# Kernel optimization log

Hardware: AMD Instinct MI355X
Metric: run time of the kernel (lower is better)

## Reference

```python
import jax, jax.numpy as jnp
import numpy as np

N_NODES = 50000
N_HYPEREDGES = 20000


def _segment_softmax(logits, seg, num_segments):
    mx = jax.ops.segment_max(logits, seg, num_segments=num_segments)
    mx = jnp.where(jnp.isfinite(mx), mx, 0.0)
    e = jnp.exp(logits - mx[seg])
    s = jax.ops.segment_sum(e, seg, num_segments=num_segments)
    return e / (s[seg] + 1e-16)


def _hypergraph_conv(x, he_node, he_edge, W, bias, num_nodes, num_he):
    # PyG HypergraphConv (use_attention=False, heads=1, hyperedge_weight=1):
    # out = D^{-1} H B^{-1} H^T (x W) + bias
    h = x @ W  # [N, C]
    ones = jnp.ones_like(he_node, dtype=h.dtype)
    D = jax.ops.segment_sum(ones, he_node, num_segments=num_nodes)
    Dinv = jnp.where(D > 0, 1.0 / D, 0.0)
    B = jax.ops.segment_sum(ones, he_edge, num_segments=num_he)
    Binv = jnp.where(B > 0, 1.0 / B, 0.0)
    # node -> hyperedge
    m = Binv[:, None] * jax.ops.segment_sum(h[he_node], he_edge, num_segments=num_he)
    # hyperedge -> node
    out = Dinv[:, None] * jax.ops.segment_sum(m[he_edge], he_node, num_segments=num_nodes)
    return out + bias


def _gat_conv(x, edge_index, W, a_src, a_dst, bias, num_nodes):
    # PyG GATConv defaults: heads=1, concat=True, slope=0.2, add_self_loops=True
    loops = jnp.arange(num_nodes)
    src = jnp.concatenate([edge_index[0], loops])
    dst = jnp.concatenate([edge_index[1], loops])
    h = x @ W  # [N, C]
    asrc = h @ a_src  # [N]
    adst = h @ a_dst  # [N]
    logit = jax.nn.leaky_relu(asrc[src] + adst[dst], negative_slope=0.2)
    alpha = _segment_softmax(logit, dst, num_nodes)  # softmax over incoming edges
    out = jax.ops.segment_sum(alpha[:, None] * h[src], dst, num_segments=num_nodes)
    return out + bias


def _mlp(e, Wm1, bm1, Wm2, bm2, Wm3, bm3, Wm4, bm4):
    # PyG MLP(128,64,3, num_layers=4) in eval mode: BN is identity at init,
    # dropout inactive -> Linear+ReLU chain, final Linear plain.
    h = jax.nn.relu(e @ Wm1 + bm1)
    h = jax.nn.relu(h @ Wm2 + bm2)
    h = jax.nn.relu(h @ Wm3 + bm3)
    return h @ Wm4 + bm4


def setup_inputs() -> dict:
    key = jax.random.key(0)
    ks = jax.random.split(key, 32)
    s = 0.05
    inp = {
        'x': jax.random.normal(ks[0], (N_NODES, 128), dtype=jnp.float32),
        'edge_index': jax.random.randint(ks[1], (2, 800000), 0, N_NODES),
        'he_node': jax.random.randint(ks[2], (400000,), 0, N_NODES),
        'he_edge': jax.random.randint(ks[3], (400000,), 0, N_HYPEREDGES),
        'edge_label_index': jax.random.randint(ks[4], (2, 100000), 0, N_NODES),
        'W1': jax.random.normal(ks[5], (128, 256)) * s,
        'b1': jnp.zeros((256,), jnp.float32),
        'W2': jax.random.normal(ks[6], (256, 256)) * s,
        'a2s': jax.random.normal(ks[7], (256,)) * s,
        'a2d': jax.random.normal(ks[8], (256,)) * s,
        'b2': jnp.zeros((256,), jnp.float32),
        'W3': jax.random.normal(ks[9], (256, 64)) * s,
        'a3s': jax.random.normal(ks[10], (64,)) * s,
        'a3d': jax.random.normal(ks[11], (64,)) * s,
        'b3': jnp.zeros((64,), jnp.float32),
        'Wm1': jax.random.normal(ks[12], (128, 64)) * s,
        'bm1': jnp.zeros((64,), jnp.float32),
        'Wm2': jax.random.normal(ks[13], (64, 64)) * s,
        'bm2': jnp.zeros((64,), jnp.float32),
        'Wm3': jax.random.normal(ks[14], (64, 64)) * s,
        'bm3': jnp.zeros((64,), jnp.float32),
        'Wm4': jax.random.normal(ks[15], (64, 3)) * s,
        'bm4': jnp.zeros((3,), jnp.float32),
    }
    return inp


def reference(x, edge_index, he_node, he_edge, edge_label_index,
              W1, b1, W2, a2s, a2d, b2, W3, a3s, a3d, b3,
              Wm1, bm1, Wm2, bm2, Wm3, bm3, Wm4, bm4):
    n = x.shape[0]
    # encode
    h = jax.nn.relu(_hypergraph_conv(x, he_node, he_edge, W1, b1, n, N_HYPEREDGES))
    h = jax.nn.relu(_gat_conv(h, edge_index, W2, a2s, a2d, b2, n))
    z = jax.nn.relu(_gat_conv(h, edge_index, W3, a3s, a3d, b3, n))
    # decode
    src, dst = edge_label_index[0], edge_label_index[1]
    edge_attr = jnp.concatenate([z[src], z[dst]], axis=-1)  # [L, 128]
    out = _mlp(edge_attr, Wm1, bm1, Wm2, bm2, Wm3, bm3, Wm4, bm4)  # [L, 3]
    out_pred = jnp.argmax(out, axis=-1)
    out_prob = jnp.take_along_axis(out, out_pred[:, None], axis=-1)[:, 0]
    return (out_pred, out_prob, out)
```

## Files before the change

### kernel.cpp

```cpp
#include <hip/hip_runtime.h>
#include <math.h>

#define NHE_CONST 20000

typedef float v4f __attribute__((ext_vector_type(4)));

__device__ __forceinline__ float lrelu(float x){ return x >= 0.f ? x : 0.2f * x; }

__global__ void k_count_all(const int* __restrict__ he_node, const int* __restrict__ he_edge, int inc,
                            const int* __restrict__ dst, int e,
                            int* cntN, int* cntHE, int* cntD){
  int i = blockIdx.x * blockDim.x + threadIdx.x;
  if (i < inc){ atomicAdd(&cntN[he_node[i]], 1); atomicAdd(&cntHE[he_edge[i]], 1); }
  if (i < e) atomicAdd(&cntD[dst[i]], 1);
}

__global__ __launch_bounds__(256) void k_scan_sums3(
    const int* __restrict__ p0, int n0, int* __restrict__ b0,
    const int* __restrict__ p1, int n1, int* __restrict__ b1,
    const int* __restrict__ p2, int n2, int* __restrict__ b2){
  const int* p; int n; int* bs;
  if (blockIdx.y == 0){ p = p0; n = n0; bs = b0; }
  else if (blockIdx.y == 1){ p = p1; n = n1; bs = b1; }
  else { p = p2; n = n2; bs = b2; }
  int nb = (n + 1023) / 1024;
  if ((int)blockIdx.x >= nb) return;
  __shared__ int sm[256];
  int base = blockIdx.x * 1024;
  int v = 0;
  for (int i = threadIdx.x; i < 1024; i += 256){
    int idx = base + i;
    v += (idx < n) ? p[idx] : 0;
  }
  sm[threadIdx.x] = v; __syncthreads();
  for (int d = 128; d > 0; d >>= 1){
    if (threadIdx.x < d) sm[threadIdx.x] += sm[threadIdx.x + d];
    __syncthreads();
  }
  if (threadIdx.x == 0) bs[blockIdx.x] = sm[0];
}

__global__ void k_scan_bsum3(int* b0, int nb0, int* b1, int nb1, int* b2, int nb2){
  int t = threadIdx.x;
  int* bs; int nb;
  if (t == 0){ bs = b0; nb = nb0; }
  else if (t == 1){ bs = b1; nb = nb1; }
  else if (t == 2){ bs = b2; nb = nb2; }
  else return;
  int acc = 0;
  for (int i = 0; i < nb; i++){ int v = bs[i]; bs[i] = acc; acc += v; }
}

__global__ __launch_bounds__(256) void k_scan_apply3(
    const int* __restrict__ c0, int n0, const int* __restrict__ s0, int* __restrict__ o0, int* __restrict__ u0,
    const int* __restrict__ c1, int n1, const int* __restrict__ s1, int* __restrict__ o1, int* __restrict__ u1,
    const int* __restrict__ c2, int n2, const int* __restrict__ s2, int* __restrict__ o2, int* __restrict__ u2){
  const int* cnt; int n; const int* bsum; int* off; int* cur;
  if (blockIdx.y == 0){ cnt = c0; n = n0; bsum = s0; off = o0; cur = u0; }
  else if (blockIdx.y == 1){ cnt = c1; n = n1; bsum = s1; off = o1; cur = u1; }
  else { cnt = c2; n = n2; bsum = s2; off = o2; cur = u2; }
  int nb = (n + 1023) / 1024;
  int b = blockIdx.x;
  if (b >= nb) return;
  __shared__ int sm[256];
  int base = b * 1024 + threadIdx.x * 4;
  int v[4];
  #pragma unroll
  for (int i = 0; i < 4; i++) v[i] = (base + i < n) ? cnt[base + i] : 0;
  int s = v[0] + v[1] + v[2] + v[3];
  sm[threadIdx.x] = s; __syncthreads();
  int x = s;
  for (int d = 1; d < 256; d <<= 1){
    int t = (threadIdx.x >= d) ? sm[threadIdx.x - d] : 0;
    __syncthreads();
    x += t; sm[threadIdx.x] = x;
    __syncthreads();
  }
  int run = x - s + bsum[b];
  #pragma unroll
  for (int i = 0; i < 4; i++){
    if (base + i < n) cur[base + i] = run;
    run += v[i];
    if (base + i < n) off[base + i + 1] = run;
  }
  if (b == 0 && threadIdx.x == 0) off[0] = 0;
}

__global__ void k_fill_all(const int* __restrict__ he_node, const int* __restrict__ he_edge, int inc,
                           const int* __restrict__ src, const int* __restrict__ dst, int e,
                           int* curN, int* curHE, int* curD,
                           int* __restrict__ nHEs, int* __restrict__ heNodes, int* __restrict__ srcIdx){
  int i = blockIdx.x * blockDim.x + threadIdx.x;
  if (i < inc){
    int nd = he_node[i], he = he_edge[i];
    int p = atomicAdd(&curHE[he], 1); heNodes[p] = nd;
    int q = atomicAdd(&curN[nd], 1);  nHEs[q]    = he;
  }
  if (i < e){ int p = atomicAdd(&curD[dst[i]], 1); srcIdx[p] = src[i]; }
}

__global__ __launch_bounds__(256) void k_gemm128_bias_relu(
    const float* __restrict__ A, const float* __restrict__ B, float* __restrict__ C,
    int M, int N, int K, const float* __restrict__ bias){
  __shared__ float As[16][132];
  __shared__ float Bs[16][128];
  int tid = threadIdx.x;
  int tn = tid & 15, tm = tid >> 4;
  int bm = blockIdx.x * 128, bn = blockIdx.y * 128;

  float acc[8][8];
  #pragma unroll
  for (int i = 0; i < 8; i++)
    #pragma unroll
    for (int j = 0; j < 8; j++) acc[i][j] = 0.f;

  int arow = tid >> 2, akc = (tid & 3) * 4;
  int brow = tid >> 4, bcol = (tid & 15) * 8;

  for (int k0 = 0; k0 < K; k0 += 16){
    #pragma unroll
    for (int h = 0; h < 2; h++){
      int r = arow + h * 64;
      int gr = bm + r;
      float4 av = (gr < M) ? *(const float4*)(A + (size_t)gr * K + k0 + akc)
                           : make_float4(0.f, 0.f, 0.f, 0.f);
      As[akc + 0][r] = av.x; As[akc + 1][r] = av.y;
      As[akc + 2][r] = av.z; As[akc + 3][r] = av.w;
    }
    const float* bp = B + (size_t)(k0 + brow) * N + bn + bcol;
    *(float4*)&Bs[brow][bcol]     = *(const float4*)bp;
    *(float4*)&Bs[brow][bcol + 4] = *(const float4*)(bp + 4);
    __syncthreads();

    #pragma unroll
    for (int k = 0; k < 16; k++){
      float4 a0 = *(const float4*)&As[k][tm * 8];
      float4 a1 = *(const float4*)&As[k][tm * 8 + 4];
      float4 b0 = *(const float4*)&Bs[k][tn * 8];
      float4 b1 = *(const float4*)&Bs[k][tn * 8 + 4];
      float a[8] = {a0.x, a0.y, a0.z, a0.w, a1.x, a1.y, a1.z, a1.w};
      float bb[8] = {b0.x, b0.y, b0.z, b0.w, b1.x, b1.y, b1.z, b1.w};
      #pragma unroll
      for (int i = 0; i < 8; i++)
        #pragma unroll
        for (int j = 0; j < 8; j++) acc[i][j] += a[i] * bb[j];
    }
    __syncthreads();
  }
  const float* bvp = bias + bn + tn * 8;
  float4 bb0 = *(const float4*)bvp;
  float4 bb1 = *(const float4*)(bvp + 4);
  float bv[8] = {bb0.x, bb0.y, bb0.z, bb0.w, bb1.x, bb1.y, bb1.z, bb1.w};
  #pragma unroll
  for (int i = 0; i < 8; i++){
    int r = bm + tm * 8 + i;
    if (r < M){
      float* cp = C + (size_t)r * N + bn + tn * 8;
      *(float4*)cp       = make_float4(fmaxf(acc[i][0]+bv[0],0.f), fmaxf(acc[i][1]+bv[1],0.f),
                                       fmaxf(acc[i][2]+bv[2],0.f), fmaxf(acc[i][3]+bv[3],0.f));
      *(float4*)(cp + 4) = make_float4(fmaxf(acc[i][4]+bv[4],0.f), fmaxf(acc[i][5]+bv[5],0.f),
                                       fmaxf(acc[i][6]+bv[6],0.f), fmaxf(acc[i][7]+bv[7],0.f));
    }
  }
}

__global__ __launch_bounds__(256) void k_gemm128_dots(
    const float* __restrict__ A, const float* __restrict__ B, float* __restrict__ C,
    int M, int N, int K, const float* __restrict__ a_s, const float* __restrict__ a_d,
    float* __restrict__ vs, float* __restrict__ vd){
  __shared__ float As[16][132];
  __shared__ float Bs[16][128];
  int tid = threadIdx.x;
  int tn = tid & 15, tm = tid >> 4;
  int bm = blockIdx.x * 128, bn = blockIdx.y * 128;

  float acc[8][8];
  #pragma unroll
  for (int i = 0; i < 8; i++)
    #pragma unroll
    for (int j = 0; j < 8; j++) acc[i][j] = 0.f;

  int arow = tid >> 2, akc = (tid & 3) * 4;
  int brow = tid >> 4, bcol = (tid & 15) * 8;

  for (int k0 = 0; k0 < K; k0 += 16){
    #pragma unroll
    for (int h = 0; h < 2; h++){
      int r = arow + h * 64;
      int gr = bm + r;
      float4 av = (gr < M) ? *(const float4*)(A + (size_t)gr * K + k0 + akc)
                           : make_float4(0.f, 0.f, 0.f, 0.f);
      As[akc + 0][r] = av.x; As[akc + 1][r] = av.y;
      As[akc + 2][r] = av.z; As[akc + 3][r] = av.w;
    }
    const float* bp = B + (size_t)(k0 + brow) * N + bn + bcol;
    *(float4*)&Bs[brow][bcol]     = *(const float4*)bp;
    *(float4*)&Bs[brow][bcol + 4] = *(const float4*)(bp + 4);
    __syncthreads();

    #pragma unroll
    for (int k = 0; k < 16; k++){
      float4 a0 = *(const float4*)&As[k][tm * 8];
      float4 a1 = *(const float4*)&As[k][tm * 8 + 4];
      float4 b0 = *(const float4*)&Bs[k][tn * 8];
      float4 b1 = *(const float4*)&Bs[k][tn * 8 + 4];
      float a[8] = {a0.x, a0.y, a0.z, a0.w, a1.x, a1.y, a1.z, a1.w};
      float bb[8] = {b0.x, b0.y, b0.z, b0.w, b1.x, b1.y, b1.z, b1.w};
      #pragma unroll
      for (int i = 0; i < 8; i++)
        #pragma unroll
        for (int j = 0; j < 8; j++) acc[i][j] += a[i] * bb[j];
    }
    __syncthreads();
  }
  #pragma unroll
  for (int i = 0; i < 8; i++){
    int r = bm + tm * 8 + i;
    if (r < M){
      float* cp = C + (size_t)r * N + bn + tn * 8;
      *(float4*)cp       = make_float4(acc[i][0], acc[i][1], acc[i][2], acc[i][3]);
      *(float4*)(cp + 4) = make_float4(acc[i][4], acc[i][5], acc[i][6], acc[i][7]);
    }
  }
  const float* asp = a_s + bn + tn * 8;
  const float* adp = a_d + bn + tn * 8;
  float4 s0 = *(const float4*)asp, s1 = *(const float4*)(asp + 4);
  float4 d0 = *(const float4*)adp, d1 = *(const float4*)(adp + 4);
  float sv[8] = {s0.x, s0.y, s0.z, s0.w, s1.x, s1.y, s1.z, s1.w};
  float dv[8] = {d0.x, d0.y, d0.z, d0.w, d1.x, d1.y, d1.z, d1.w};
  #pragma unroll
  for (int i = 0; i < 8; i++){
    float ps = 0.f, pd = 0.f;
    #pragma unroll
    for (int j = 0; j < 8; j++){ ps = fmaf(acc[i][j], sv[j], ps); pd = fmaf(acc[i][j], dv[j], pd); }
    ps += __shfl_xor(ps, 1); ps += __shfl_xor(ps, 2); ps += __shfl_xor(ps, 4); ps += __shfl_xor(ps, 8);
    pd += __shfl_xor(pd, 1); pd += __shfl_xor(pd, 2); pd += __shfl_xor(pd, 4); pd += __shfl_xor(pd, 8);
    int r = bm + tm * 8 + i;
    if (tn == 0 && r < M){ atomicAdd(&vs[r], ps); atomicAdd(&vd[r], pd); }
  }
}

__global__ __launch_bounds__(256) void k_gemm64_dots(
    const float* __restrict__ A, const float* __restrict__ B, float* __restrict__ C,
    int M, int N, int K, const float* __restrict__ a_s, const float* __restrict__ a_d,
    float* __restrict__ vs, float* __restrict__ vd){
  __shared__ float As[16][132];
  __shared__ float Bs[16][64];
  int tid = threadIdx.x;
  int tn = tid & 15, tm = tid >> 4;
  int bm = blockIdx.x * 128;

  float acc[8][4];
  #pragma unroll
  for (int i = 0; i < 8; i++)
    #pragma unroll
    for (int j = 0; j < 4; j++) acc[i][j] = 0.f;

  int arow = tid >> 2, akc = (tid & 3) * 4;
  int brow = tid >> 4, bcol = (tid & 15) * 4;

  for (int k0 = 0; k0 < K; k0 += 16){
    #pragma unroll
    for (int h = 0; h < 2; h++){
      int r = arow + h * 64;
      int gr = bm + r;
      float4 av = (gr < M) ? *(const float4*)(A + (size_t)gr * K + k0 + akc)
                           : make_float4(0.f, 0.f, 0.f, 0.f);
      As[akc + 0][r] = av.x; As[akc + 1][r] = av.y;
      As[akc + 2][r] = av.z; As[akc + 3][r] = av.w;
    }
    *(float4*)&Bs[brow][bcol] = *(const float4*)(B + (size_t)(k0 + brow) * N + bcol);
    __syncthreads();

    #pragma unroll
    for (int k = 0; k < 16; k++){
      float4 a0 = *(const float4*)&As[k][tm * 8];
      float4 a1 = *(const float4*)&As[k][tm * 8 + 4];
      float4 b  = *(const float4*)&Bs[k][tn * 4];
      float a[8] = {a0.x, a0.y, a0.z, a0.w, a1.x, a1.y, a1.z, a1.w};
      float bb[4] = {b.x, b.y, b.z, b.w};
      #pragma unroll
      for (int i = 0; i < 8; i++)
        #pragma unroll
        for (int j = 0; j < 4; j++) acc[i][j] += a[i] * bb[j];
    }
    __syncthreads();
  }
  float4 s = *(const float4*)(a_s + tn * 4);
  float4 d = *(const float4*)(a_d + tn * 4);
  #pragma unroll
  for (int i = 0; i < 8; i++){
    int r = bm + tm * 8 + i;
    if (r < M)
      *(float4*)(C + (size_t)r * N + tn * 4) = make_float4(acc[i][0], acc[i][1], acc[i][2], acc[i][3]);
    float ps = acc[i][0]*s.x + acc[i][1]*s.y + acc[i][2]*s.z + acc[i][3]*s.w;
    float pd = acc[i][0]*d.x + acc[i][1]*d.y + acc[i][2]*d.z + acc[i][3]*d.w;
    ps += __shfl_xor(ps, 1); ps += __shfl_xor(ps, 2); ps += __shfl_xor(ps, 4); ps += __shfl_xor(ps, 8);
    pd += __shfl_xor(pd, 1); pd += __shfl_xor(pd, 2); pd += __shfl_xor(pd, 4); pd += __shfl_xor(pd, 8);
    if (tn == 0 && r < M){ vs[r] = ps; vd[r] = pd; }
  }
}

__global__ __launch_bounds__(256) void k_hg_edge128(const float* __restrict__ x, const int* __restrict__ off,
                                                    const int* __restrict__ heNodes, float* __restrict__ mout,
                                                    int nhe){
  int wid = (blockIdx.x * blockDim.x + threadIdx.x) >> 6;
  int lane = threadIdx.x & 63;
  if (wid >= nhe) return;
  int s = off[wid], e = off[wid + 1];
  float2 a0 = make_float2(0,0), a1 = a0, a2 = a0, a3 = a0;
  int i = s;
  for (; i + 8 <= e; i += 8){
    int n8[8];
    #pragma unroll
    for (int u = 0; u < 8; u++) n8[u] = heNodes[i + u];
    float2 v8[8];
    #pragma unroll
    for (int u = 0; u < 8; u++) v8[u] = *(const float2*)(x + (size_t)n8[u] * 128 + lane * 2);
    #pragma unroll
    for (int u = 0; u < 8; u++){
      float2* c = (u & 3) == 0 ? &a0 : (u & 3) == 1 ? &a1 : (u & 3) == 2 ? &a2 : &a3;
      c->x += v8[u].x; c->y += v8[u].y;
    }
  }
  for (; i < e; i++){
    int nd = heNodes[i];
    float2 v = *(const float2*)(x + (size_t)nd * 128 + lane * 2);
    a0.x += v.x; a0.y += v.y;
  }
  float inv = (e > s) ? 1.f / (float)(e - s) : 0.f;
  float2 o = make_float2((a0.x + a1.x + a2.x + a3.x) * inv, (a0.y + a1.y + a2.y + a3.y) * inv);
  *(float2*)(mout + (size_t)wid * 128 + lane * 2) = o;
}

__global__ __launch_bounds__(256) void k_hg_node128(const float* __restrict__ m_in, const int* __restrict__ off,
                                                    const int* __restrict__ nHEs, float* __restrict__ out,
                                                    int nn){
  int wid = (blockIdx.x * blockDim.x + threadIdx.x) >> 6;
  int lane = threadIdx.x & 63;
  if (wid >= nn) return;
  int s = off[wid], e = off[wid + 1];
  float2 a0 = make_float2(0,0), a1 = a0, a2 = a0, a3 = a0;
  int i = s;
  for (; i + 4 <= e; i += 4){
    int n0 = nHEs[i], n1 = nHEs[i+1], n2 = nHEs[i+2], n3 = nHEs[i+3];
    float2 v0 = *(const float2*)(m_in + (size_t)n0 * 128 + lane * 2);
    float2 v1 = *(const float2*)(m_in + (size_t)n1 * 128 + lane * 2);
    float2 v2 = *(const float2*)(m_in + (size_t)n2 * 128 + lane * 2);
    float2 v3 = *(const float2*)(m_in + (size_t)n3 * 128 + lane * 2);
    a0.x += v0.x; a0.y += v0.y; a1.x += v1.x; a1.y += v1.y;
    a2.x += v2.x; a2.y += v2.y; a3.x += v3.x; a3.y += v3.y;
  }
  for (; i < e; i++){
    int he = nHEs[i];
    float2 v = *(const float2*)(m_in + (size_t)he * 128 + lane * 2);
    a0.x += v.x; a0.y += v.y;
  }
  float inv = (e > s) ? 1.f / (float)(e - s) : 0.f;
  float2 o = make_float2((a0.x + a1.x + a2.x + a3.x) * inv, (a0.y + a1.y + a2.y + a3.y) * inv);
  *(float2*)(out + (size_t)wid * 128 + lane * 2) = o;
}

__global__ __launch_bounds__(256) void k_gat256(const float* __restrict__ h, const float* __restrict__ asr,
                                                const float* __restrict__ ads, const int* __restrict__ off,
                                                const int* __restrict__ srcIdx, const float* __restrict__ bias,
                                                float* __restrict__ out, int nn){
  int wid = (blockIdx.x * blockDim.x + threadIdx.x) >> 6;
  int lane = threadIdx.x & 63;
  if (wid >= nn) return;
  float ad = ads[wid];
  int s = off[wid], e = off[wid + 1];

  float ssum = 0.f;
  float4 c0 = make_float4(0,0,0,0), c1 = c0, c2 = c0, c3 = c0;
  {
    float e0 = __expf(lrelu(asr[wid] + ad));
    ssum += e0;
    float4 v = *(const float4*)(h + (size_t)wid * 256 + lane * 4);
    c0.x += e0 * v.x; c0.y += e0 * v.y; c0.z += e0 * v.z; c0.w += e0 * v.w;
  }
  int i = s;
  for (; i + 8 <= e; i += 8){
    int n8[8];
    #pragma unroll
    for (int u = 0; u < 8; u++) n8[u] = srcIdx[i + u];
    float f8[8];
    #pragma unroll
    for (int u = 0; u < 8; u++) f8[u] = asr[n8[u]];
    float4 v8[8];
    #pragma unroll
    for (int u = 0; u < 8; u++) v8[u] = *(const float4*)(h + (size_t)n8[u] * 256 + lane * 4);
    #pragma unroll
    for (int u = 0; u < 8; u++){
      float ee = __expf(lrelu(f8[u] + ad));
      ssum += ee;
      float4* c = (u & 3) == 0 ? &c0 : (u & 3) == 1 ? &c1 : (u & 3) == 2 ? &c2 : &c3;
      c->x += ee * v8[u].x; c->y += ee * v8[u].y; c->z += ee * v8[u].z; c->w += ee * v8[u].w;
    }
  }
  for (; i < e; i++){
    int sn = srcIdx[i];
    float ee = __expf(lrelu(asr[sn] + ad));
    ssum += ee;
    float4 v = *(const float4*)(h + (size_t)sn * 256 + lane * 4);
    c0.x += ee * v.x; c0.y += ee * v.y; c0.z += ee * v.z; c0.w += ee * v.w;
  }
  float r = 1.f / (ssum + 1e-16f);
  float4 b = *(const float4*)(bias + lane * 4);
  v4f o;
  o.x = fmaxf((c0.x + c1.x + c2.x + c3.x) * r + b.x, 0.f);
  o.y = fmaxf((c0.y + c1.y + c2.y + c3.y) * r + b.y, 0.f);
  o.z = fmaxf((c0.z + c1.z + c2.z + c3.z) * r + b.z, 0.f);
  o.w = fmaxf((c0.w + c1.w + c2.w + c3.w) * r + b.w, 0.f);
  __builtin_nontemporal_store(o, (v4f*)(out + (size_t)wid * 256 + lane * 4));
}

__global__ __launch_bounds__(256) void k_gat64(const float* __restrict__ h, const float* __restrict__ asr,
                                               const float* __restrict__ ads, const int* __restrict__ off,
                                               const int* __restrict__ srcIdx, const float* __restrict__ bias,
                                               float* __restrict__ out, int nn){
  int wid = (blockIdx.x * blockDim.x + threadIdx.x) >> 6;
  int lane = threadIdx.x & 63;
  if (wid >= nn) return;
  float ad = ads[wid];
  int s = off[wid], e = off[wid + 1];

  float ssum = 0.f;
  float c0 = 0.f, c1 = 0.f, c2 = 0.f, c3 = 0.f;
  {
    float e0 = __expf(lrelu(asr[wid] + ad));
    ssum += e0;
    c0 += e0 * h[(size_t)wid * 64 + lane];
  }
  int i = s;
  for (; i + 8 <= e; i += 8){
    int n8[8];
    #pragma unroll
    for (int u = 0; u < 8; u++) n8[u] = srcIdx[i + u];
    float f8[8], v8[8];
    #pragma unroll
    for (int u = 0; u < 8; u++) f8[u] = asr[n8[u]];
    #pragma unroll
    for (int u = 0; u < 8; u++) v8[u] = h[(size_t)n8[u] * 64 + lane];
    #pragma unroll
    for (int u = 0; u < 8; u++){
      float ee = __expf(lrelu(f8[u] + ad));
      ssum += ee;
      if ((u & 3) == 0) c0 += ee * v8[u];
      else if ((u & 3) == 1) c1 += ee * v8[u];
      else if ((u & 3) == 2) c2 += ee * v8[u];
      else c3 += ee * v8[u];
    }
  }
  for (; i < e; i++){
    int sn = srcIdx[i];
    float ee = __expf(lrelu(asr[sn] + ad));
    ssum += ee;
    c0 += ee * h[(size_t)sn * 64 + lane];
  }
  float r = 1.f / (ssum + 1e-16f);
  out[(size_t)wid * 64 + lane] = fmaxf((c0 + c1 + c2 + c3) * r + bias[lane], 0.f);
}

#define DEC_EPB 128

__device__ __forceinline__ void dec_stageW(float (*Ws)[68], const float* __restrict__ W, int tid){
  #pragma unroll
  for (int i = 0; i < 4; i++){
    int idx = tid + i * 256;
    int r = idx >> 4, c = (idx & 15) * 4;
    *(float4*)&Ws[r][c] = *(const float4*)(W + r * 64 + c);
  }
}

__device__ __forceinline__ void dec_gather(float (*act)[132], const float* __restrict__ z,
                                           const int* __restrict__ idxv, int ebase, int wv, int lane, int L){
  #pragma unroll 4
  for (int t = 0; t < 32; t++){
    int le = wv * 32 + t;
    int e = ebase + le;
    int nd = (e < L) ? idxv[e] : 0;
    act[lane][le] = z[(size_t)nd * 64 + lane];
  }
}

__device__ __forceinline__ void dec_mac64(const float (*act)[132], const float (*Ws)[68],
                                          int tm, int tn, float (&acc)[8][4]){
  #pragma unroll 8
  for (int k = 0; k < 64; k++){
    float4 a0 = *(const float4*)&act[k][tm * 8];
    float4 a1 = *(const float4*)&act[k][tm * 8 + 4];
    float4 b  = *(const float4*)&Ws[k][tn * 4];
    float a[8] = {a0.x, a0.y, a0.z, a0.w, a1.x, a1.y, a1.z, a1.w};
    #pragma unroll
    for (int i = 0; i < 8; i++){
      acc[i][0] = fmaf(a[i], b.x, acc[i][0]);
      acc[i][1] = fmaf(a[i], b.y, acc[i][1]);
      acc[i][2] = fmaf(a[i], b.z, acc[i][2]);
      acc[i][3] = fmaf(a[i], b.w, acc[i][3]);
    }
  }
}

__device__ __forceinline__ void dec_writeback(float (*act)[132], int tm, int tn, const float (&acc)[8][4]){
  #pragma unroll
  for (int j = 0; j < 4; j++)
    #pragma unroll
    for (int i = 0; i < 8; i++)
      act[tn * 4 + j][tm * 8 + i] = fmaxf(acc[i][j], 0.f);
}

__global__ __launch_bounds__(256) void k_decode(const float* __restrict__ z, const int* __restrict__ eli, int L,
    const float* __restrict__ Wm1, const float* __restrict__ bm1,
    const float* __restrict__ Wm2, const float* __restrict__ bm2,
    const float* __restrict__ Wm3, const float* __restrict__ bm3,
    const float* __restrict__ Wm4, const float* __restrict__ bm4,
    float* __restrict__ outPred, float* __restrict__ outProb, float* __restrict__ outLog){
  __shared__ float act[64][132];
  __shared__ float Ws[64][68];
  __shared__ float W4s[192];
  __shared__ float b1s[64], b2s[64], b3s[64], b4s[4];

  int tid = threadIdx.x, lane = tid & 63, wv = tid >> 6;
  int tm = tid >> 4, tn = tid & 15;
  int ebase = blockIdx.x * DEC_EPB;

  if (tid < 64){ b1s[tid] = bm1[tid]; b2s[tid] = bm2[tid]; b3s[tid] = bm3[tid]; }
  if (tid < 3) b4s[tid] = bm4[tid];
  if (tid < 192) W4s[tid] = Wm4[tid];

  dec_stageW(Ws, Wm1, tid);
  dec_gather(act, z, eli, ebase, wv, lane, L);
  __syncthreads();

  float acc[8][4];
  {
    float bx = b1s[tn*4], by = b1s[tn*4+1], bz = b1s[tn*4+2], bw = b1s[tn*4+3];
    #pragma unroll
    for (int i = 0; i < 8; i++){ acc[i][0]=bx; acc[i][1]=by; acc[i][2]=bz; acc[i][3]=bw; }
  }
  dec_mac64(act, Ws, tm, tn, acc);
  __syncthreads();

  dec_stageW(Ws, Wm1 + 4096, tid);
  dec_gather(act, z, eli + L, ebase, wv, lane, L);
  __syncthreads();
  dec_mac64(act, Ws, tm, tn, acc);
  __syncthreads();

  dec_writeback(act, tm, tn, acc);
  dec_stageW(Ws, Wm2, tid);
  __syncthreads();

  {
    float bx = b2s[tn*4], by = b2s[tn*4+1], bz = b2s[tn*4+2], bw = b2s[tn*4+3];
    #pragma unroll
    for (int i = 0; i < 8; i++){ acc[i][0]=bx; acc[i][1]=by; acc[i][2]=bz; acc[i][3]=bw; }
  }
  dec_mac64(act, Ws, tm, tn, acc);
  __syncthreads();
  dec_writeback(act, tm, tn, acc);
  dec_stageW(Ws, Wm3, tid);
  __syncthreads();

  {
    float bx = b3s[tn*4], by = b3s[tn*4+1], bz = b3s[tn*4+2], bw = b3s[tn*4+3];
    #pragma unroll
    for (int i = 0; i < 8; i++){ acc[i][0]=bx; acc[i][1]=by; acc[i][2]=bz; acc[i][3]=bw; }
  }
  dec_mac64(act, Ws, tm, tn, acc);
  __syncthreads();
  dec_writeback(act, tm, tn, acc);
  __syncthreads();

  if (tid < DEC_EPB){
    int e = tid;
    float o0 = b4s[0], o1 = b4s[1], o2 = b4s[2];
    #pragma unroll 8
    for (int k = 0; k < 64; k++){
      float av = act[k][e];
      o0 = fmaf(av, W4s[k*3+0], o0);
      o1 = fmaf(av, W4s[k*3+1], o1);
      o2 = fmaf(av, W4s[k*3+2], o2);
    }
    int eg = ebase + e;
    if (eg < L){
      int am = 0; float best = o0;
      if (o1 > best){ am = 1; best = o1; }
      if (o2 > best){ am = 2; best = o2; }
      outPred[eg] = (float)am;
      outProb[eg] = best;
      outLog[(size_t)eg * 3 + 0] = o0;
      outLog[(size_t)eg * 3 + 1] = o1;
      outLog[(size_t)eg * 3 + 2] = o2;
    }
  }
}

extern "C" void kernel_launch(void* const* d_in, const int* in_sizes, int n_in,
                              void* d_out, int out_size, void* d_ws, size_t ws_size,
                              hipStream_t stream){
  const float* x      = (const float*)d_in[0];
  const int*   ei     = (const int*)d_in[1];
  const int*   he_node= (const int*)d_in[2];
  const int*   he_edge= (const int*)d_in[3];
  const int*   eli    = (const int*)d_in[4];
  const float* W1  = (const float*)d_in[5];
  const float* b1  = (const float*)d_in[6];
  const float* W2  = (const float*)d_in[7];
  const float* a2s = (const float*)d_in[8];
  const float* a2d = (const float*)d_in[9];
  const float* b2  = (const float*)d_in[10];
  const float* W3  = (const float*)d_in[11];
  const float* a3s = (const float*)d_in[12];
  const float* a3d = (const float*)d_in[13];
  const float* b3  = (const float*)d_in[14];
  const float* Wm1 = (const float*)d_in[15]; const float* bm1 = (const float*)d_in[16];
  const float* Wm2 = (const float*)d_in[17]; const float* bm2 = (const float*)d_in[18];
  const float* Wm3 = (const float*)d_in[19]; const float* bm3 = (const float*)d_in[20];
  const float* Wm4 = (const float*)d_in[21]; const float* bm4 = (const float*)d_in[22];

  const int N   = in_sizes[0] / 128;
  const int E   = in_sizes[1] / 2;
  const int INC = in_sizes[2];
  const int NHE = NHE_CONST;
  const int L   = in_sizes[4] / 2;

  char* wbase = (char*)d_ws;
  size_t woff = 0;
  auto walloc = [&](size_t bytes) -> void* {
    void* p = wbase + woff;
    woff = (woff + bytes + 255) & ~(size_t)255;
    return p;
  };
  float* pre1   = (float*)walloc((size_t)N * 128 * 4);
  float* mbuf   = (float*)walloc((size_t)NHE * 128 * 4);
  float* h1     = (float*)walloc((size_t)N * 256 * 4);
  float* t2     = (float*)walloc((size_t)N * 256 * 4);
  float* t3     = (float*)walloc((size_t)N * 64 * 4);
  float* zbuf   = (float*)walloc((size_t)N * 64 * 4);
  float* vboth  = (float*)walloc((size_t)2 * N * 4);
  int* heOff  = (int*)walloc((size_t)(NHE + 1) * 4);
  int* nOff   = (int*)walloc((size_t)(N + 1) * 4);
  int* dOff   = (int*)walloc((size_t)(N + 1) * 4);
  int* cntAll = (int*)walloc((size_t)(NHE + 2 * N) * 4);
  int* curAll = (int*)walloc((size_t)(NHE + 2 * N) * 4);
  int* heNodes= (int*)walloc((size_t)INC * 4);
  int* nHEs   = (int*)walloc((size_t)INC * 4);
  int* srcIdx = (int*)walloc((size_t)E * 4);
  int* bsumA  = (int*)walloc(64 * 4);
  int* bsumB  = (int*)walloc(64 * 4);
  int* bsumC  = (int*)walloc(64 * 4);

  int* cntHE = cntAll;           int* cntN = cntAll + NHE; int* cntD = cntAll + NHE + N;
  int* curHE = curAll;           int* curN = curAll + NHE; int* curD = curAll + NHE + N;
  float* vsrc = vboth;           float* vdst = vboth + N;
  float* h2 = h1;

  const int* srcPtr = ei;
  const int* dstPtr = ei + E;

  hipMemsetAsync(cntAll, 0, (size_t)(NHE + 2 * N) * 4, stream);
  hipMemsetAsync(vboth,  0, (size_t)2 * N * 4, stream);
  k_count_all<<<(E + 255) / 256, 256, 0, stream>>>(he_node, he_edge, INC, dstPtr, E, cntN, cntHE, cntD);

  int nbHE = (NHE + 1023) / 1024;
  int nbN  = (N + 1023) / 1024;
  k_scan_sums3<<<dim3(nbN, 3), 256, 0, stream>>>(cntHE, NHE, bsumA, cntN, N, bsumB, cntD, N, bsumC);
  k_scan_bsum3<<<1, 64, 0, stream>>>(bsumA, nbHE, bsumB, nbN, bsumC, nbN);
  k_scan_apply3<<<dim3(nbN, 3), 256, 0, stream>>>(cntHE, NHE, bsumA, heOff, curHE,
                                                  cntN,  N,   bsumB, nOff,  curN,
                                                  cntD,  N,   bsumC, dOff,  curD);
  k_fill_all<<<(E + 255) / 256, 256, 0, stream>>>(he_node, he_edge, INC, srcPtr, dstPtr, E,
                                                  curN, curHE, curD, nHEs, heNodes, srcIdx);

  int gRowA = (N + 127) / 128;
  int gWav  = (N + 3) / 4;

  k_hg_edge128<<<(NHE + 3) / 4, 256, 0, stream>>>(x, heOff, heNodes, mbuf, NHE);
  k_hg_node128<<<gWav, 256, 0, stream>>>(mbuf, nOff, nHEs, pre1, N);
  k_gemm128_bias_relu<<<dim3(gRowA, 2), 256, 0, stream>>>(pre1, W1, h1, N, 256, 128, b1);

  k_gemm128_dots<<<dim3(gRowA, 2), 256, 0, stream>>>(h1, W2, t2, N, 256, 256, a2s, a2d, vsrc, vdst);
  k_gat256<<<gWav, 256, 0, stream>>>(t2, vsrc, vdst, dOff, srcIdx, b2, h2, N);

  k_gemm64_dots<<<dim3(gRowA, 1), 256, 0, stream>>>(h2, W3, t3, N, 64, 256, a3s, a3d, vsrc, vdst);
  k_gat64<<<gWav, 256, 0, stream>>>(t3, vsrc, vdst, dOff, srcIdx, b3, zbuf, N);

  float* outPred = (float*)d_out;
  float* outProb = outPred + L;
  float* outLog  = outProb + L;
  k_decode<<<(L + DEC_EPB - 1) / DEC_EPB, 256, 0, stream>>>(zbuf, eli, L,
                                    Wm1, bm1, Wm2, bm2, Wm3, bm3, Wm4, bm4,
                                    outPred, outProb, outLog);
}
```

Measured before the change: 848.0 us.

## Slice CSR fill by destination range so each block targets one eighth of buckets

Replaces the one-thread-per-edge fill kernel with a grid of 8 slices times 128 groups. Each slice grid-strides over all edges but only handles those whose destination node or hyperedge falls in its eighth of the id range. The aim is to confine atomics and scattered writes to a smaller working set per block, so they get better L2 locality and less contention. In exchange every edge index is read eight times, which adds read traffic.

```diff
diff --git a/kernel.cpp b/kernel.cpp
--- a/kernel.cpp
+++ b/kernel.cpp
@@ -86,17 +86,37 @@
   if (b == 0 && threadIdx.x == 0) off[0] = 0;
 }
 
-__global__ void k_fill_all(const int* __restrict__ he_node, const int* __restrict__ he_edge, int inc,
-                           const int* __restrict__ src, const int* __restrict__ dst, int e,
-                           int* curN, int* curHE, int* curD,
-                           int* __restrict__ nHEs, int* __restrict__ heNodes, int* __restrict__ srcIdx){
-  int i = blockIdx.x * blockDim.x + threadIdx.x;
-  if (i < inc){
+__global__ __launch_bounds__(256) void k_fill_sliced(
+    const int* __restrict__ he_node, const int* __restrict__ he_edge, int inc,
+    const int* __restrict__ src, const int* __restrict__ dst, int e,
+    int* curN, int* curHE, int* curD,
+    int* __restrict__ nHEs, int* __restrict__ heNodes, int* __restrict__ srcIdx,
+    int nN, int nHE){
+  int slice = blockIdx.x & 7;
+  int group = blockIdx.x >> 3;
+  int ngroups = gridDim.x >> 3;
+  int sN  = (nN  + 7) >> 3;  int loN  = slice * sN;  int hiN  = min(loN + sN, nN);
+  int sHE = (nHE + 7) >> 3;  int loHE = slice * sHE; int hiHE = min(loHE + sHE, nHE);
+  int stride = ngroups * 256;
+  int start = group * 256 + threadIdx.x;
+  for (int i = start; i < e; i += stride){
+    int d = dst[i];
+    if (d >= loN && d < hiN){
+      int p = atomicAdd(&curD[d], 1);
+      srcIdx[p] = src[i];
+    }
+  }
+  for (int i = start; i < inc; i += stride){
     int nd = he_node[i], he = he_edge[i];
-    int p = atomicAdd(&curHE[he], 1); heNodes[p] = nd;
-    int q = atomicAdd(&curN[nd], 1);  nHEs[q]    = he;
-  }
-  if (i < e){ int p = atomicAdd(&curD[dst[i]], 1); srcIdx[p] = src[i]; }
+    if (nd >= loN && nd < hiN){
+      int q = atomicAdd(&curN[nd], 1);
+      nHEs[q] = he;
+    }
+    if (he >= loHE && he < hiHE){
+      int p = atomicAdd(&curHE[he], 1);
+      heNodes[p] = nd;
+    }
+  }
 }
 
 __global__ __launch_bounds__(256) void k_gemm128_bias_relu(
@@ -671,8 +691,8 @@
   k_scan_apply3<<<dim3(nbN, 3), 256, 0, stream>>>(cntHE, NHE, bsumA, heOff, curHE,
                                                   cntN,  N,   bsumB, nOff,  curN,
                                                   cntD,  N,   bsumC, dOff,  curD);
-  k_fill_all<<<(E + 255) / 256, 256, 0, stream>>>(he_node, he_edge, INC, srcPtr, dstPtr, E,
-                                                  curN, curHE, curD, nHEs, heNodes, srcIdx);
+  k_fill_sliced<<<8 * 128, 256, 0, stream>>>(he_node, he_edge, INC, srcPtr, dstPtr, E,
+                                             curN, curHE, curD, nHEs, heNodes, srcIdx, N, NHE);
 
   int gRowA = (N + 127) / 128;
   int gWav  = (N + 3) / 4;
```

Result: faster. 803.7 us (-5.2%).
